# Kernel tuning notes

Measured on AMD Instinct MI355X. Metric: run time of the kernel, lower is better.

Reference implementation:

```python
import jax, jax.numpy as jnp
import numpy as np

N_USERS = 100_000
N_ITEMS = 50_000
N_EDGES = 2_000_000
D = 64
ALPHA = 0.5      # tanh-blend coefficient (alpha)
NORM_2 = -1.0    # exponent on back-aggregation degree norm (args.norm_2)


def setup_inputs() -> dict:
    key = jax.random.key(0)
    k1, k2, k3, k4, k5 = jax.random.split(key, 5)
    return {
        "h_user": jax.random.normal(k1, (N_USERS, D), jnp.float32) * 0.1,
        "pretrained_feature": jax.random.normal(k2, (N_ITEMS, D), jnp.float32),
        "edge_w": jax.random.normal(k3, (N_ITEMS, 1), jnp.float32),
        "src_idx": jax.random.randint(k4, (N_EDGES,), 0, N_USERS, dtype=jnp.int32),
        "dst_idx": jax.random.randint(k5, (N_EDGES,), 0, N_ITEMS, dtype=jnp.int32),
    }


def reference(h_user, pretrained_feature, edge_w, src_idx, dst_idx):
    # HGCNLayer.forward: bidirectional copy_src+sum aggregation with degree norm,
    # tanh prompt blend and node-softmax edge weighting.
    ones = jnp.ones((N_EDGES,), h_user.dtype)

    # forward pass user -> item: rst[d] = sum_{(s,d) in E} h_user[s]
    rst = jax.ops.segment_sum(h_user[src_idx], dst_idx, num_segments=N_ITEMS)  # [N_ITEMS, D]
    deg_dst = jnp.clip(jax.ops.segment_sum(ones, dst_idx, num_segments=N_ITEMS), 1.0)

    # alpha * tanh prompt blend
    rst = rst + ALPHA * jnp.tanh(pretrained_feature)
    # edge-prompt softmax scaling (softmax over nodes; see notes)
    rst = jax.nn.softmax(edge_w, axis=0) * rst
    # in-degree^-1 normalization
    rst = rst / deg_dst[:, None]

    # backward pass item -> user: bsrc[s] = sum_{(s,d) in E} rst[d]
    bsrc = jax.ops.segment_sum(rst[dst_idx], src_idx, num_segments=N_USERS)  # [N_USERS, D]
    deg_src = jnp.clip(jax.ops.segment_sum(ones, src_idx, num_segments=N_USERS), 1.0)
    bsrc = bsrc * jnp.power(deg_src, NORM_2)[:, None]
    return bsrc
```

## Files before the change

### kernel.cpp

```cpp
#include <hip/hip_runtime.h>
#include <hip/hip_bf16.h>
#include <math.h>

#define N_USERS 100000
#define N_ITEMS 50000
#define N_EDGES 2000000
#define D 64

#define FB_BINS 98
#define BB_BINS 196
#define NBINS   (FB_BINS + BB_BINS)
#define CHUNK   2048
#define NCHUNK  ((N_EDGES + CHUNK - 1) / CHUNK)
#define FINE_FWD (FB_BINS * 512)
#define FINE_ALL (FINE_FWD + BB_BINS * 512)
#define FWD_WGS ((N_ITEMS + 31) / 32)
#define BWD_WGS ((N_USERS + 31) / 32)

__device__ __forceinline__ float blo(unsigned u) {
    union { unsigned i; float f; } c; c.i = u << 16; return c.f;
}
__device__ __forceinline__ float bhi(unsigned u) {
    union { unsigned i; float f; } c; c.i = u & 0xFFFF0000u; return c.f;
}
__device__ __forceinline__ unsigned bpack(float x, float y) {
    __hip_bfloat16 a = __float2bfloat16(x), b = __float2bfloat16(y);
    unsigned short ua = *reinterpret_cast<unsigned short*>(&a);
    unsigned short ub = *reinterpret_cast<unsigned short*>(&b);
    return (unsigned)ua | ((unsigned)ub << 16);
}

__global__ __launch_bounds__(256) void h2b_kernel(
    const float2* __restrict__ in, unsigned* __restrict__ out, int n) {
    int stride = gridDim.x * blockDim.x;
    for (int i = blockIdx.x * blockDim.x + threadIdx.x; i < n; i += stride) {
        float2 v = in[i];
        out[i] = bpack(v.x, v.y);
    }
}

__global__ __launch_bounds__(256) void hist_kernel(
    const int* __restrict__ src, const int* __restrict__ dst, int* __restrict__ gh) {
    __shared__ int h[NBINS];
    for (int i = threadIdx.x; i < NBINS; i += 256) h[i] = 0;
    __syncthreads();
    int stride = gridDim.x * blockDim.x;
    for (int e = blockIdx.x * blockDim.x + threadIdx.x; e < N_EDGES; e += stride) {
        atomicAdd(&h[dst[e] >> 9], 1);
        atomicAdd(&h[FB_BINS + (src[e] >> 9)], 1);
    }
    __syncthreads();
    for (int i = threadIdx.x; i < NBINS; i += 256) {
        int v = h[i];
        if (v) atomicAdd(&gh[i], v);
    }
}

__global__ void scan_excl(const int* __restrict__ in, int* __restrict__ out,
                          int* __restrict__ cur, int n) {
    const int T = 1024, E = 4;
    __shared__ int wsum[16];
    __shared__ int s_carry;
    if (threadIdx.x == 0) s_carry = 0;
    __syncthreads();

    int lane = threadIdx.x & 63;
    int wid  = threadIdx.x >> 6;

    for (int base = 0; base < n; base += T * E) {
        int idx0 = base + threadIdx.x * E;
        int v[E];
        int tot = 0;
#pragma unroll
        for (int e = 0; e < E; e++) {
            int i = idx0 + e;
            v[e] = (i < n) ? in[i] : 0;
            tot += v[e];
        }
        int incl = tot;
#pragma unroll
        for (int off = 1; off < 64; off <<= 1) {
            int t = __shfl_up(incl, off);
            if (lane >= off) incl += t;
        }
        if (lane == 63) wsum[wid] = incl;
        __syncthreads();
        if (wid == 0 && lane < 16) {
            int t = wsum[lane];
            int sc = t;
#pragma unroll
            for (int off = 1; off < 16; off <<= 1) {
                int u = __shfl_up(sc, off);
                if (lane >= off) sc += u;
            }
            wsum[lane] = sc - t;
        }
        __syncthreads();
        int wave_off = wsum[wid];
        int excl = s_carry + wave_off + incl - tot;
#pragma unroll
        for (int e = 0; e < E; e++) {
            int i = idx0 + e;
            if (i < n) { out[i] = excl; cur[i] = excl; }
            excl += v[e];
        }
        __syncthreads();
        if (threadIdx.x == T - 1) s_carry += wave_off + incl;
        __syncthreads();
    }
    if (threadIdx.x == 0) out[n] = s_carry;
}

__global__ __launch_bounds__(256) void binfill_kernel(
    const int* __restrict__ src, const int* __restrict__ dst,
    int* __restrict__ gcur, unsigned* __restrict__ stage) {
    __shared__ int cnt[NBINS];
    __shared__ int gbase[NBINS];
    __shared__ int lcur[NBINS];
    int c = blockIdx.x;
    int base = c * CHUNK;
    int nEdge = N_EDGES - base; if (nEdge > CHUNK) nEdge = CHUNK;

    for (int t = threadIdx.x; t < NBINS; t += 256) { cnt[t] = 0; lcur[t] = 0; }
    __syncthreads();

    int es[8], ed[8];
#pragma unroll
    for (int j = 0; j < 8; j++) {
        int k = j * 256 + threadIdx.x;
        if (k < nEdge) {
            es[j] = src[base + k];
            ed[j] = dst[base + k];
            atomicAdd(&cnt[ed[j] >> 9], 1);
            atomicAdd(&cnt[FB_BINS + (es[j] >> 9)], 1);
        } else {
            es[j] = -1;
        }
    }
    __syncthreads();
    for (int t = threadIdx.x; t < NBINS; t += 256) {
        int cv = cnt[t];
        gbase[t] = cv ? atomicAdd(&gcur[t], cv) : 0;
    }
    __syncthreads();
#pragma unroll
    for (int j = 0; j < 8; j++) {
        if (es[j] >= 0) {
            int s = es[j], d = ed[j];
            int bf = d >> 9;
            int p = atomicAdd(&lcur[bf], 1);
            stage[gbase[bf] + p] = (unsigned)s | ((unsigned)(d & 511) << 17);
            int bb = FB_BINS + (s >> 9);
            int q = atomicAdd(&lcur[bb], 1);
            stage[gbase[bb] + q] = (unsigned)d | ((unsigned)(s & 511) << 16);
        }
    }
}

__global__ __launch_bounds__(512) void redist_kernel(
    const unsigned* __restrict__ stage, const int* __restrict__ binoff,
    unsigned* __restrict__ stage2, int* __restrict__ fineoff) {
    __shared__ int cnt[512];
    __shared__ int wsum[8];
    int B = blockIdx.x;
    int fwd = (B < FB_BINS) ? 1 : 0;
    int beg = binoff[B], end = binoff[B + 1];
    int tid = threadIdx.x, lane = tid & 63, wv = tid >> 6;
    int sh = fwd ? 17 : 16;
    unsigned pmask = fwd ? 0x1FFFFu : 0xFFFFu;

    cnt[tid] = 0;
    __syncthreads();
    for (int k = beg + tid; k < end; k += 512)
        atomicAdd(&cnt[(stage[k] >> sh) & 511], 1);
    __syncthreads();

    int v = cnt[tid];
    int incl = v;
#pragma unroll
    for (int off = 1; off < 64; off <<= 1) {
        int t = __shfl_up(incl, off);
        if (lane >= off) incl += t;
    }
    if (lane == 63) wsum[wv] = incl;
    __syncthreads();
    if (tid == 0) {
        int run = 0;
#pragma unroll
        for (int w = 0; w < 8; w++) { int t = wsum[w]; wsum[w] = run; run += t; }
    }
    __syncthreads();
    int excl = wsum[wv] + incl - v;

    int fbase = fwd ? (B * 512) : (FINE_FWD + (B - FB_BINS) * 512);
    fineoff[fbase + tid] = beg + excl;
    cnt[tid] = excl;
    __syncthreads();

    for (int k = beg + tid; k < end; k += 512) {
        unsigned e = stage[k];
        int lid = (e >> sh) & 511;
        int p = atomicAdd(&cnt[lid], 1);
        stage2[beg + p] = e & pmask;
    }
}

__global__ void softmax_stats_kernel(const float* __restrict__ w, float* __restrict__ stats) {
    __shared__ float red[16];
    int tid = threadIdx.x, lane = tid & 63, wid = tid >> 6;

    float m = -INFINITY;
    for (int i = tid; i < N_ITEMS; i += 1024) m = fmaxf(m, w[i]);
#pragma unroll
    for (int off = 32; off; off >>= 1) m = fmaxf(m, __shfl_xor(m, off));
    if (lane == 0) red[wid] = m;
    __syncthreads();
    if (tid == 0) {
        float t = red[0];
        for (int k = 1; k < 16; k++) t = fmaxf(t, red[k]);
        red[0] = t;
    }
    __syncthreads();
    m = red[0];
    __syncthreads();

    float s = 0.f;
    for (int i = tid; i < N_ITEMS; i += 1024) s += expf(w[i] - m);
#pragma unroll
    for (int off = 32; off; off >>= 1) s += __shfl_xor(s, off);
    if (lane == 0) red[wid] = s;
    __syncthreads();
    if (tid == 0) {
        float t = 0.f;
        for (int k = 0; k < 16; k++) t += red[k];
        stats[0] = m;
        stats[1] = t;
    }
}

__global__ __launch_bounds__(256) void pass2_fwd_kernel(
    const unsigned* __restrict__ hu16, const float* __restrict__ pf,
    const float* __restrict__ edge_w, const unsigned* __restrict__ stage2,
    const int* __restrict__ fineoff, const float* __restrict__ stats,
    unsigned* __restrict__ rst16) {
    int tid = threadIdx.x, lane = tid & 63, wv = tid >> 6;
    int q = lane & 31, half = lane >> 5;
    float m = stats[0], ssum = stats[1];
    const float2* PF2 = (const float2*)pf;
    int i0 = blockIdx.x * 32;

    for (int il = wv; il < 32; il += 4) {
        int i = i0 + il;
        if (i >= N_ITEMS) break;
        int a = fineoff[i], b = fineoff[i + 1];
        float ax = 0.f, ay = 0.f;
        int k = a;
        for (; k + 8 <= b; k += 8) {
            int s0 = (int)stage2[k + half],     s1 = (int)stage2[k + 2 + half];
            int s2 = (int)stage2[k + 4 + half], s3 = (int)stage2[k + 6 + half];
            unsigned u0 = hu16[(s0 << 5) + q];
            unsigned u1 = hu16[(s1 << 5) + q];
            unsigned u2 = hu16[(s2 << 5) + q];
            unsigned u3 = hu16[(s3 << 5) + q];
            ax += (blo(u0) + blo(u1)) + (blo(u2) + blo(u3));
            ay += (bhi(u0) + bhi(u1)) + (bhi(u2) + bhi(u3));
        }
        for (; k + 2 <= b; k += 2) {
            unsigned u = hu16[((int)stage2[k + half] << 5) + q];
            ax += blo(u); ay += bhi(u);
        }
        if (k < b && half == 0) {
            unsigned u = hu16[((int)stage2[k] << 5) + q];
            ax += blo(u); ay += bhi(u);
        }
        ax += __shfl_xor(ax, 32);
        ay += __shfl_xor(ay, 32);
        if (half == 0) {
            float deg = (float)(b - a);
            if (deg < 1.f) deg = 1.f;
            float sc = expf(edge_w[i] - m) / (ssum * deg);
            float2 pv = PF2[(size_t)i * 32 + q];
            float vx = (ax + 0.5f * tanhf(pv.x)) * sc;
            float vy = (ay + 0.5f * tanhf(pv.y)) * sc;
            rst16[(size_t)i * 32 + q] = bpack(vx, vy);
        }
    }
}

__global__ __launch_bounds__(256) void pass2_bwd_kernel(
    const unsigned* __restrict__ rst16, const unsigned* __restrict__ stage2,
    const int* __restrict__ fineoff, float* __restrict__ out) {
    int tid = threadIdx.x, lane = tid & 63, wv = tid >> 6;
    int q = lane & 31, half = lane >> 5;
    float2* OUT2 = (float2*)out;
    int u0i = blockIdx.x * 32;

    for (int il = wv; il < 32; il += 4) {
        int u = u0i + il;
        if (u >= N_USERS) break;
        int a = fineoff[FINE_FWD + u], b = fineoff[FINE_FWD + u + 1];
        float ax = 0.f, ay = 0.f;
        int k = a;
        for (; k + 8 <= b; k += 8) {
            int d0 = (int)stage2[k + half],     d1 = (int)stage2[k + 2 + half];
            int d2 = (int)stage2[k + 4 + half], d3 = (int)stage2[k + 6 + half];
            unsigned u0 = rst16[(d0 << 5) + q];
            unsigned u1 = rst16[(d1 << 5) + q];
            unsigned u2 = rst16[(d2 << 5) + q];
            unsigned u3 = rst16[(d3 << 5) + q];
            ax += (blo(u0) + blo(u1)) + (blo(u2) + blo(u3));
            ay += (bhi(u0) + bhi(u1)) + (bhi(u2) + bhi(u3));
        }
        for (; k + 2 <= b; k += 2) {
            unsigned e = rst16[((int)stage2[k + half] << 5) + q];
            ax += blo(e); ay += bhi(e);
        }
        if (k < b && half == 0) {
            unsigned e = rst16[((int)stage2[k] << 5) + q];
            ax += blo(e); ay += bhi(e);
        }
        ax += __shfl_xor(ax, 32);
        ay += __shfl_xor(ay, 32);
        if (half == 0) {
            float deg = (float)(b - a);
            if (deg < 1.f) deg = 1.f;
            OUT2[(size_t)u * 32 + q] = make_float2(ax / deg, ay / deg);
        }
    }
}

extern "C" void kernel_launch(void* const* d_in, const int* in_sizes, int n_in,
                              void* d_out, int out_size, void* d_ws, size_t ws_size,
                              hipStream_t stream) {
    const float* h_user = (const float*)d_in[0];
    const float* pf     = (const float*)d_in[1];
    const float* edge_w = (const float*)d_in[2];
    const int*   src    = (const int*)d_in[3];
    const int*   dst    = (const int*)d_in[4];
    float* out = (float*)d_out;

    char* p = (char*)d_ws;
    int* gh      = (int*)p;      p += sizeof(int) * NBINS;
    int* binoff  = (int*)p;      p += sizeof(int) * (NBINS + 1);
    int* gcur    = (int*)p;      p += sizeof(int) * NBINS;
    int* fineoff = (int*)p;      p += sizeof(int) * FINE_ALL;
    unsigned* stage  = (unsigned*)p; p += sizeof(unsigned) * (size_t)2 * N_EDGES;
    unsigned* stage2 = (unsigned*)p; p += sizeof(unsigned) * (size_t)2 * N_EDGES;
    unsigned* hu16   = (unsigned*)p; p += sizeof(unsigned) * (size_t)N_USERS * 32;
    unsigned* rst16  = (unsigned*)p; p += sizeof(unsigned) * (size_t)N_ITEMS * 32;
    float* stats = (float*)p;    p += 2 * sizeof(float);

    hipMemsetAsync(gh, 0, sizeof(int) * NBINS, stream);

    hist_kernel<<<256, 256, 0, stream>>>(src, dst, gh);
    scan_excl<<<1, 1024, 0, stream>>>(gh, binoff, gcur, NBINS);
    binfill_kernel<<<NCHUNK, 256, 0, stream>>>(src, dst, gcur, stage);
    redist_kernel<<<NBINS, 512, 0, stream>>>(stage, binoff, stage2, fineoff);
    h2b_kernel<<<1024, 256, 0, stream>>>((const float2*)h_user, hu16, N_USERS * 32);
    softmax_stats_kernel<<<1, 1024, 0, stream>>>(edge_w, stats);
    pass2_fwd_kernel<<<FWD_WGS, 256, 0, stream>>>(hu16, pf, edge_w, stage2, fineoff, stats, rst16);
    pass2_bwd_kernel<<<BWD_WGS, 256, 0, stream>>>(rst16, stage2, fineoff, out);
}
```

Before: 350.2 us.

## Build CSR via global per-node degree histogram and multi-block scan

Replaces the coarse bin histogram and the per-bin shared-memory redistribution with a global per-node degree count, computed with atomics and fused into the bf16 conversion kernel. A three-stage multi-block scan then produces the fine offsets directly. The redistribution kernel is split four ways per bin and uses global atomics on per-node cursors, which gives more parallelism than one workgroup per bin. The softmax stats are folded into the scan kernel, cutting launch count. The cost is heavy global atomic traffic on 150K counters in the prep pass and a large memset.

Measured after the change: 528.5 us. +50.9%, slower.

```diff
diff --git a/kernel.cpp b/kernel.cpp
--- a/kernel.cpp
+++ b/kernel.cpp
@@ -10,10 +10,15 @@
 #define FB_BINS 98
 #define BB_BINS 196
 #define NBINS   (FB_BINS + BB_BINS)
+#define NBINS_P8 296
 #define CHUNK   2048
 #define NCHUNK  ((N_EDGES + CHUNK - 1) / CHUNK)
 #define FINE_FWD (FB_BINS * 512)
-#define FINE_ALL (FINE_FWD + BB_BINS * 512)
+#define FINE_TOT (NBINS * 512)
+#define SCAN_BLK 4096
+#define SCAN_WGS 37
+#define FINE_PAD (SCAN_WGS * SCAN_BLK)
+#define TOTSLOT  (2 * N_EDGES)
 #define FWD_WGS ((N_ITEMS + 31) / 32)
 #define BWD_WGS ((N_USERS + 31) / 32)
 
@@ -30,85 +35,127 @@
     return (unsigned)ua | ((unsigned)ub << 16);
 }
 
-__global__ __launch_bounds__(256) void h2b_kernel(
-    const float2* __restrict__ in, unsigned* __restrict__ out, int n) {
+__global__ __launch_bounds__(256) void prep_kernel(
+    const float2* __restrict__ hin, unsigned* __restrict__ hu16,
+    const int* __restrict__ src, const int* __restrict__ dst,
+    int* __restrict__ deg) {
     int stride = gridDim.x * blockDim.x;
-    for (int i = blockIdx.x * blockDim.x + threadIdx.x; i < n; i += stride) {
-        float2 v = in[i];
-        out[i] = bpack(v.x, v.y);
-    }
-}
-
-__global__ __launch_bounds__(256) void hist_kernel(
-    const int* __restrict__ src, const int* __restrict__ dst, int* __restrict__ gh) {
-    __shared__ int h[NBINS];
-    for (int i = threadIdx.x; i < NBINS; i += 256) h[i] = 0;
-    __syncthreads();
-    int stride = gridDim.x * blockDim.x;
-    for (int e = blockIdx.x * blockDim.x + threadIdx.x; e < N_EDGES; e += stride) {
-        atomicAdd(&h[dst[e] >> 9], 1);
-        atomicAdd(&h[FB_BINS + (src[e] >> 9)], 1);
-    }
-    __syncthreads();
-    for (int i = threadIdx.x; i < NBINS; i += 256) {
-        int v = h[i];
-        if (v) atomicAdd(&gh[i], v);
-    }
-}
-
-__global__ void scan_excl(const int* __restrict__ in, int* __restrict__ out,
-                          int* __restrict__ cur, int n) {
-    const int T = 1024, E = 4;
-    __shared__ int wsum[16];
-    __shared__ int s_carry;
-    if (threadIdx.x == 0) s_carry = 0;
-    __syncthreads();
-
-    int lane = threadIdx.x & 63;
-    int wid  = threadIdx.x >> 6;
-
-    for (int base = 0; base < n; base += T * E) {
-        int idx0 = base + threadIdx.x * E;
-        int v[E];
-        int tot = 0;
-#pragma unroll
-        for (int e = 0; e < E; e++) {
-            int i = idx0 + e;
-            v[e] = (i < n) ? in[i] : 0;
-            tot += v[e];
-        }
-        int incl = tot;
-#pragma unroll
-        for (int off = 1; off < 64; off <<= 1) {
-            int t = __shfl_up(incl, off);
-            if (lane >= off) incl += t;
-        }
-        if (lane == 63) wsum[wid] = incl;
-        __syncthreads();
-        if (wid == 0 && lane < 16) {
-            int t = wsum[lane];
-            int sc = t;
-#pragma unroll
-            for (int off = 1; off < 16; off <<= 1) {
-                int u = __shfl_up(sc, off);
-                if (lane >= off) sc += u;
+    int t0 = blockIdx.x * blockDim.x + threadIdx.x;
+    for (int i = t0; i < N_USERS * 32; i += stride) {
+        float2 v = hin[i];
+        hu16[i] = bpack(v.x, v.y);
+    }
+    for (int e = t0; e < N_EDGES; e += stride) {
+        atomicAdd(&deg[dst[e]], 1);
+        atomicAdd(&deg[FINE_FWD + src[e]], 1);
+    }
+}
+
+__global__ __launch_bounds__(256) void scanA_kernel(
+    const int* __restrict__ deg, int* __restrict__ blocksum) {
+    __shared__ int ws[4];
+    int b = blockIdx.x, t = threadIdx.x, lane = t & 63, wv = t >> 6;
+    const int4* Dp = (const int4*)(deg + b * SCAN_BLK);
+    int s = 0;
+#pragma unroll
+    for (int j = 0; j < 4; j++) {
+        int4 v = Dp[t * 4 + j];
+        s += v.x + v.y + v.z + v.w;
+    }
+#pragma unroll
+    for (int off = 32; off; off >>= 1) s += __shfl_xor(s, off);
+    if (lane == 0) ws[wv] = s;
+    __syncthreads();
+    if (t == 0) blocksum[b] = ws[0] + ws[1] + ws[2] + ws[3];
+}
+
+__global__ void scanB_kernel(const int* __restrict__ blocksum, int* __restrict__ blockbase,
+                             const float* __restrict__ w, float* __restrict__ stats) {
+    __shared__ float red[16];
+    if (blockIdx.x == 0) {
+        int t = threadIdx.x;
+        if (t < 64) {
+            int v = (t < SCAN_WGS) ? blocksum[t] : 0;
+            int incl = v;
+#pragma unroll
+            for (int off = 1; off < 64; off <<= 1) {
+                int u = __shfl_up(incl, off);
+                if (t >= off) incl += u;
             }
-            wsum[lane] = sc - t;
-        }
-        __syncthreads();
-        int wave_off = wsum[wid];
-        int excl = s_carry + wave_off + incl - tot;
-#pragma unroll
-        for (int e = 0; e < E; e++) {
-            int i = idx0 + e;
-            if (i < n) { out[i] = excl; cur[i] = excl; }
-            excl += v[e];
-        }
-        __syncthreads();
-        if (threadIdx.x == T - 1) s_carry += wave_off + incl;
-        __syncthreads();
-    }
-    if (threadIdx.x == 0) out[n] = s_carry;
+            if (t < SCAN_WGS) blockbase[t] = incl - v;
+        }
+        return;
+    }
+    int tid = threadIdx.x, lane = tid & 63, wid = tid >> 6;
+
+    float m = -INFINITY;
+    for (int i = tid; i < N_ITEMS; i += 1024) m = fmaxf(m, w[i]);
+#pragma unroll
+    for (int off = 32; off; off >>= 1) m = fmaxf(m, __shfl_xor(m, off));
+    if (lane == 0) red[wid] = m;
+    __syncthreads();
+    if (tid == 0) {
+        float t = red[0];
+        for (int k = 1; k < 16; k++) t = fmaxf(t, red[k]);
+        red[0] = t;
+    }
+    __syncthreads();
+    m = red[0];
+    __syncthreads();
+
+    float s = 0.f;
+    for (int i = tid; i < N_ITEMS; i += 1024) s += expf(w[i] - m);
+#pragma unroll
+    for (int off = 32; off; off >>= 1) s += __shfl_xor(s, off);
+    if (lane == 0) red[wid] = s;
+    __syncthreads();
+    if (tid == 0) {
+        float t = 0.f;
+        for (int k = 0; k < 16; k++) t += red[k];
+        stats[0] = m;
+        stats[1] = t;
+    }
+}
+
+__global__ __launch_bounds__(256) void scanC_kernel(
+    const int* __restrict__ blockbase, int* deg_cur,
+    int* __restrict__ fineoff, int* __restrict__ gcur) {
+    __shared__ int wbase[4];
+    int b = blockIdx.x, t = threadIdx.x, lane = t & 63, wv = t >> 6;
+    int4 v[4];
+    const int4* Dp = (const int4*)(deg_cur + b * SCAN_BLK);
+#pragma unroll
+    for (int j = 0; j < 4; j++) v[j] = Dp[t * 4 + j];
+    int tot = 0;
+#pragma unroll
+    for (int j = 0; j < 4; j++) tot += v[j].x + v[j].y + v[j].z + v[j].w;
+    int incl = tot;
+#pragma unroll
+    for (int off = 1; off < 64; off <<= 1) {
+        int u = __shfl_up(incl, off);
+        if (lane >= off) incl += u;
+    }
+    if (lane == 63) wbase[wv] = incl;
+    __syncthreads();
+    if (t == 0) {
+        int run = 0;
+#pragma unroll
+        for (int k = 0; k < 4; k++) { int x = wbase[k]; wbase[k] = run; run += x; }
+    }
+    __syncthreads();
+    int base = blockbase[b] + wbase[wv] + incl - tot;
+    int idx0 = b * SCAN_BLK + t * 16;
+#pragma unroll
+    for (int j = 0; j < 4; j++) {
+        int c0 = v[j].x, c1 = v[j].y, c2 = v[j].z, c3 = v[j].w;
+        int i = idx0 + j * 4;
+        fineoff[i] = base; deg_cur[i] = base;
+        if ((i & 511) == 0 && (i >> 9) < NBINS) gcur[i >> 9] = base;
+        base += c0;
+        fineoff[i + 1] = base; deg_cur[i + 1] = base; base += c1;
+        fineoff[i + 2] = base; deg_cur[i + 2] = base; base += c2;
+        fineoff[i + 3] = base; deg_cur[i + 3] = base; base += c3;
+    }
 }
 
 __global__ __launch_bounds__(256) void binfill_kernel(
@@ -157,84 +204,30 @@
     }
 }
 
-__global__ __launch_bounds__(512) void redist_kernel(
-    const unsigned* __restrict__ stage, const int* __restrict__ binoff,
-    unsigned* __restrict__ stage2, int* __restrict__ fineoff) {
-    __shared__ int cnt[512];
-    __shared__ int wsum[8];
-    int B = blockIdx.x;
-    int fwd = (B < FB_BINS) ? 1 : 0;
-    int beg = binoff[B], end = binoff[B + 1];
-    int tid = threadIdx.x, lane = tid & 63, wv = tid >> 6;
-    int sh = fwd ? 17 : 16;
-    unsigned pmask = fwd ? 0x1FFFFu : 0xFFFFu;
-
-    cnt[tid] = 0;
-    __syncthreads();
-    for (int k = beg + tid; k < end; k += 512)
-        atomicAdd(&cnt[(stage[k] >> sh) & 511], 1);
-    __syncthreads();
-
-    int v = cnt[tid];
-    int incl = v;
-#pragma unroll
-    for (int off = 1; off < 64; off <<= 1) {
-        int t = __shfl_up(incl, off);
-        if (lane >= off) incl += t;
-    }
-    if (lane == 63) wsum[wv] = incl;
-    __syncthreads();
-    if (tid == 0) {
-        int run = 0;
-#pragma unroll
-        for (int w = 0; w < 8; w++) { int t = wsum[w]; wsum[w] = run; run += t; }
-    }
-    __syncthreads();
-    int excl = wsum[wv] + incl - v;
-
-    int fbase = fwd ? (B * 512) : (FINE_FWD + (B - FB_BINS) * 512);
-    fineoff[fbase + tid] = beg + excl;
-    cnt[tid] = excl;
-    __syncthreads();
-
-    for (int k = beg + tid; k < end; k += 512) {
-        unsigned e = stage[k];
-        int lid = (e >> sh) & 511;
-        int p = atomicAdd(&cnt[lid], 1);
-        stage2[beg + p] = e & pmask;
-    }
-}
-
-__global__ void softmax_stats_kernel(const float* __restrict__ w, float* __restrict__ stats) {
-    __shared__ float red[16];
-    int tid = threadIdx.x, lane = tid & 63, wid = tid >> 6;
-
-    float m = -INFINITY;
-    for (int i = tid; i < N_ITEMS; i += 1024) m = fmaxf(m, w[i]);
-#pragma unroll
-    for (int off = 32; off; off >>= 1) m = fmaxf(m, __shfl_xor(m, off));
-    if (lane == 0) red[wid] = m;
-    __syncthreads();
-    if (tid == 0) {
-        float t = red[0];
-        for (int k = 1; k < 16; k++) t = fmaxf(t, red[k]);
-        red[0] = t;
-    }
-    __syncthreads();
-    m = red[0];
-    __syncthreads();
-
-    float s = 0.f;
-    for (int i = tid; i < N_ITEMS; i += 1024) s += expf(w[i] - m);
-#pragma unroll
-    for (int off = 32; off; off >>= 1) s += __shfl_xor(s, off);
-    if (lane == 0) red[wid] = s;
-    __syncthreads();
-    if (tid == 0) {
-        float t = 0.f;
-        for (int k = 0; k < 16; k++) t += red[k];
-        stats[0] = m;
-        stats[1] = t;
+__global__ __launch_bounds__(256) void redist2_kernel(
+    const unsigned* __restrict__ stage, const int* __restrict__ fineoff,
+    int* __restrict__ cur, unsigned* __restrict__ stage2) {
+    int x = blockIdx.x;
+    int B = x % NBINS_P8, s4 = x / NBINS_P8;
+    if (B >= NBINS) return;
+    int beg = fineoff[B << 9], end = fineoff[(B + 1) << 9];
+    int n = end - beg;
+    int q0 = beg + ((n * s4) >> 2), q1 = beg + ((n * (s4 + 1)) >> 2);
+    int t = threadIdx.x;
+    if (B < FB_BINS) {
+        for (int k = q0 + t; k < q1; k += 256) {
+            unsigned e = stage[k];
+            int gid = (B << 9) | (int)(e >> 17);
+            int p = atomicAdd(&cur[gid], 1);
+            stage2[p] = e & 0x1FFFFu;
+        }
+    } else {
+        for (int k = q0 + t; k < q1; k += 256) {
+            unsigned e = stage[k];
+            int gid = (B << 9) | (int)(e >> 16);
+            int p = atomicAdd(&cur[gid], 1);
+            stage2[p] = e & 0xFFFFu;
+        }
     }
 }
 
@@ -340,24 +333,25 @@
     float* out = (float*)d_out;
 
     char* p = (char*)d_ws;
-    int* gh      = (int*)p;      p += sizeof(int) * NBINS;
-    int* binoff  = (int*)p;      p += sizeof(int) * (NBINS + 1);
-    int* gcur    = (int*)p;      p += sizeof(int) * NBINS;
-    int* fineoff = (int*)p;      p += sizeof(int) * FINE_ALL;
-    unsigned* stage  = (unsigned*)p; p += sizeof(unsigned) * (size_t)2 * N_EDGES;
-    unsigned* stage2 = (unsigned*)p; p += sizeof(unsigned) * (size_t)2 * N_EDGES;
+    int* deg      = (int*)p;     p += sizeof(int) * FINE_PAD;
+    int* fineoff  = (int*)p;     p += sizeof(int) * FINE_PAD;
+    int* gcur     = (int*)p;     p += sizeof(int) * NBINS_P8;
+    int* blocksum = (int*)p;     p += sizeof(int) * 64;
+    int* blockbase= (int*)p;     p += sizeof(int) * 64;
+    unsigned* stage  = (unsigned*)p; p += sizeof(unsigned) * (size_t)TOTSLOT;
+    unsigned* stage2 = (unsigned*)p; p += sizeof(unsigned) * (size_t)TOTSLOT;
     unsigned* hu16   = (unsigned*)p; p += sizeof(unsigned) * (size_t)N_USERS * 32;
     unsigned* rst16  = (unsigned*)p; p += sizeof(unsigned) * (size_t)N_ITEMS * 32;
-    float* stats = (float*)p;    p += 2 * sizeof(float);
-
-    hipMemsetAsync(gh, 0, sizeof(int) * NBINS, stream);
-
-    hist_kernel<<<256, 256, 0, stream>>>(src, dst, gh);
-    scan_excl<<<1, 1024, 0, stream>>>(gh, binoff, gcur, NBINS);
+    float* stats = (float*)p;    p += 4 * sizeof(float);
+
+    hipMemsetAsync(deg, 0, sizeof(int) * FINE_PAD, stream);
+
+    prep_kernel<<<1024, 256, 0, stream>>>((const float2*)h_user, hu16, src, dst, deg);
+    scanA_kernel<<<SCAN_WGS, 256, 0, stream>>>(deg, blocksum);
+    scanB_kernel<<<2, 1024, 0, stream>>>(blocksum, blockbase, edge_w, stats);
+    scanC_kernel<<<SCAN_WGS, 256, 0, stream>>>(blockbase, deg, fineoff, gcur);
     binfill_kernel<<<NCHUNK, 256, 0, stream>>>(src, dst, gcur, stage);
-    redist_kernel<<<NBINS, 512, 0, stream>>>(stage, binoff, stage2, fineoff);
-    h2b_kernel<<<1024, 256, 0, stream>>>((const float2*)h_user, hu16, N_USERS * 32);
-    softmax_stats_kernel<<<1, 1024, 0, stream>>>(edge_w, stats);
+    redist2_kernel<<<4 * NBINS_P8, 256, 0, stream>>>(stage, fineoff, deg, stage2);
     pass2_fwd_kernel<<<FWD_WGS, 256, 0, stream>>>(hu16, pf, edge_w, stage2, fineoff, stats, rst16);
     pass2_bwd_kernel<<<BWD_WGS, 256, 0, stream>>>(rst16, stage2, fineoff, out);
 }
```

## Split forward gather into source-sharded partial sums with a combine pass

Applied to the files above, without the earlier changes.

The forward user-to-item aggregation now sub-buckets each item's edges by the low two bits of the source index. Four separate workgroup groups each gather one shard into bf16 partial buffers, and a second kernel combines the partials and applies the tanh blend, softmax scale and degree normalisation. The redistribution kernel is reworked to build these sharded offsets, and the backward bins are processed two per workgroup. Index stream loads become nontemporal. The aim is better cache locality on the user embedding gathers, at the cost of an extra kernel, partial-sum traffic and an added bf16 rounding of the partials.

Result: slower. 398.1 us (+13.7%).

```diff
diff --git a/kernel.cpp b/kernel.cpp
--- a/kernel.cpp
+++ b/kernel.cpp
@@ -12,9 +12,13 @@
 #define NBINS   (FB_BINS + BB_BINS)
 #define CHUNK   2048
 #define NCHUNK  ((N_EDGES + CHUNK - 1) / CHUNK)
-#define FINE_FWD (FB_BINS * 512)
-#define FINE_ALL (FINE_FWD + BB_BINS * 512)
-#define FWD_WGS ((N_ITEMS + 31) / 32)
+#define NSH     4
+#define FOFF_F_N (FB_BINS * 512 * NSH + 1)
+#define FOFF_B_N (BB_BINS * 512 + 1)
+#define TOTSLOT  (2 * N_EDGES)
+#define PART_SLOTS (FB_BINS * 512 * NSH)
+#define PASSA_WGS (((N_ITEMS + 31) / 32) * 8)
+#define PASSB_WGS ((N_ITEMS + 7) / 8)
 #define BWD_WGS ((N_USERS + 31) / 32)
 
 __device__ __forceinline__ float blo(unsigned u) {
@@ -157,51 +161,94 @@
     }
 }
 
-__global__ __launch_bounds__(512) void redist_kernel(
+__global__ __launch_bounds__(512) void redist3_kernel(
     const unsigned* __restrict__ stage, const int* __restrict__ binoff,
-    unsigned* __restrict__ stage2, int* __restrict__ fineoff) {
-    __shared__ int cnt[512];
+    unsigned* __restrict__ stage2, int* __restrict__ foff_f, int* __restrict__ foff_b) {
+    __shared__ int cnt[512 * NSH];
     __shared__ int wsum[8];
-    int B = blockIdx.x;
-    int fwd = (B < FB_BINS) ? 1 : 0;
-    int beg = binoff[B], end = binoff[B + 1];
-    int tid = threadIdx.x, lane = tid & 63, wv = tid >> 6;
-    int sh = fwd ? 17 : 16;
-    unsigned pmask = fwd ? 0x1FFFFu : 0xFFFFu;
-
-    cnt[tid] = 0;
-    __syncthreads();
-    for (int k = beg + tid; k < end; k += 512)
-        atomicAdd(&cnt[(stage[k] >> sh) & 511], 1);
-    __syncthreads();
-
-    int v = cnt[tid];
-    int incl = v;
-#pragma unroll
-    for (int off = 1; off < 64; off <<= 1) {
-        int t = __shfl_up(incl, off);
-        if (lane >= off) incl += t;
-    }
-    if (lane == 63) wsum[wv] = incl;
-    __syncthreads();
-    if (tid == 0) {
-        int run = 0;
-#pragma unroll
-        for (int w = 0; w < 8; w++) { int t = wsum[w]; wsum[w] = run; run += t; }
-    }
-    __syncthreads();
-    int excl = wsum[wv] + incl - v;
-
-    int fbase = fwd ? (B * 512) : (FINE_FWD + (B - FB_BINS) * 512);
-    fineoff[fbase + tid] = beg + excl;
-    cnt[tid] = excl;
-    __syncthreads();
-
-    for (int k = beg + tid; k < end; k += 512) {
-        unsigned e = stage[k];
-        int lid = (e >> sh) & 511;
-        int p = atomicAdd(&cnt[lid], 1);
-        stage2[beg + p] = e & pmask;
+    int wg = blockIdx.x, t = threadIdx.x, lane = t & 63, wv = t >> 6;
+
+    if (wg < FB_BINS) {
+        int B = wg;
+        int beg = binoff[B], end = binoff[B + 1];
+        for (int j = t; j < 512 * NSH; j += 512) cnt[j] = 0;
+        __syncthreads();
+        for (int k = beg + t; k < end; k += 512) {
+            unsigned e = stage[k];
+            atomicAdd(&cnt[(((e >> 17) & 511) << 2) | (e & 3)], 1);
+        }
+        __syncthreads();
+        int c[NSH]; int tot = 0;
+#pragma unroll
+        for (int j = 0; j < NSH; j++) { c[j] = cnt[(t << 2) | j]; tot += c[j]; }
+        int incl = tot;
+#pragma unroll
+        for (int off = 1; off < 64; off <<= 1) {
+            int u = __shfl_up(incl, off);
+            if (lane >= off) incl += u;
+        }
+        if (lane == 63) wsum[wv] = incl;
+        __syncthreads();
+        if (t == 0) {
+            int run = 0;
+#pragma unroll
+            for (int k2 = 0; k2 < 8; k2++) { int x = wsum[k2]; wsum[k2] = run; run += x; }
+        }
+        __syncthreads();
+        int base = beg + wsum[wv] + incl - tot;
+        int slot0 = (((B << 9) | t) << 2);
+#pragma unroll
+        for (int j = 0; j < NSH; j++) {
+            foff_f[slot0 + j] = base;
+            cnt[(t << 2) | j] = base;
+            base += c[j];
+        }
+        if (B == FB_BINS - 1 && t == 0) foff_f[FB_BINS * 512 * NSH] = end;
+        __syncthreads();
+        for (int k = beg + t; k < end; k += 512) {
+            unsigned e = stage[k];
+            int idx = (((e >> 17) & 511) << 2) | (e & 3);
+            int p = atomicAdd(&cnt[idx], 1);
+            stage2[p] = e & 0x1FFFFu;
+        }
+    } else {
+        for (int pass = 0; pass < 2; pass++) {
+            int B = FB_BINS + ((wg - FB_BINS) << 1) + pass;
+            int beg = binoff[B], end = binoff[B + 1];
+            cnt[t] = 0;
+            __syncthreads();
+            for (int k = beg + t; k < end; k += 512) {
+                unsigned e = stage[k];
+                atomicAdd(&cnt[(e >> 16) & 511], 1);
+            }
+            __syncthreads();
+            int v = cnt[t];
+            int incl = v;
+#pragma unroll
+            for (int off = 1; off < 64; off <<= 1) {
+                int u = __shfl_up(incl, off);
+                if (lane >= off) incl += u;
+            }
+            if (lane == 63) wsum[wv] = incl;
+            __syncthreads();
+            if (t == 0) {
+                int run = 0;
+#pragma unroll
+                for (int k2 = 0; k2 < 8; k2++) { int x = wsum[k2]; wsum[k2] = run; run += x; }
+            }
+            __syncthreads();
+            int base = beg + wsum[wv] + incl - v;
+            foff_b[((B - FB_BINS) << 9) | t] = base;
+            cnt[t] = base;
+            if (B == NBINS - 1 && t == 0) foff_b[BB_BINS * 512] = end;
+            __syncthreads();
+            for (int k = beg + t; k < end; k += 512) {
+                unsigned e = stage[k];
+                int p = atomicAdd(&cnt[(e >> 16) & 511], 1);
+                stage2[p] = e & 0xFFFFu;
+            }
+            __syncthreads();
+        }
     }
 }
 
@@ -238,26 +285,27 @@
     }
 }
 
-__global__ __launch_bounds__(256) void pass2_fwd_kernel(
-    const unsigned* __restrict__ hu16, const float* __restrict__ pf,
-    const float* __restrict__ edge_w, const unsigned* __restrict__ stage2,
-    const int* __restrict__ fineoff, const float* __restrict__ stats,
-    unsigned* __restrict__ rst16) {
+__global__ __launch_bounds__(256) void passA_fwd_kernel(
+    const unsigned* __restrict__ hu16, const unsigned* __restrict__ stage2,
+    const int* __restrict__ foff_f, unsigned* __restrict__ part) {
     int tid = threadIdx.x, lane = tid & 63, wv = tid >> 6;
     int q = lane & 31, half = lane >> 5;
-    float m = stats[0], ssum = stats[1];
-    const float2* PF2 = (const float2*)pf;
-    int i0 = blockIdx.x * 32;
-
-    for (int il = wv; il < 32; il += 4) {
+    int ib = blockIdx.x >> 3, x = blockIdx.x & 7;
+    int sh = x >> 1, hb = x & 1;
+    int i0 = ib * 32 + hb * 16;
+
+    for (int il = wv; il < 16; il += 4) {
         int i = i0 + il;
         if (i >= N_ITEMS) break;
-        int a = fineoff[i], b = fineoff[i + 1];
+        int slot = (i << 2) | sh;
+        int a = foff_f[slot], b = foff_f[slot + 1];
         float ax = 0.f, ay = 0.f;
         int k = a;
         for (; k + 8 <= b; k += 8) {
-            int s0 = (int)stage2[k + half],     s1 = (int)stage2[k + 2 + half];
-            int s2 = (int)stage2[k + 4 + half], s3 = (int)stage2[k + 6 + half];
+            int s0 = (int)__builtin_nontemporal_load(&stage2[k + half]);
+            int s1 = (int)__builtin_nontemporal_load(&stage2[k + 2 + half]);
+            int s2 = (int)__builtin_nontemporal_load(&stage2[k + 4 + half]);
+            int s3 = (int)__builtin_nontemporal_load(&stage2[k + 6 + half]);
             unsigned u0 = hu16[(s0 << 5) + q];
             unsigned u1 = hu16[(s1 << 5) + q];
             unsigned u2 = hu16[(s2 << 5) + q];
@@ -266,30 +314,48 @@
             ay += (bhi(u0) + bhi(u1)) + (bhi(u2) + bhi(u3));
         }
         for (; k + 2 <= b; k += 2) {
-            unsigned u = hu16[((int)stage2[k + half] << 5) + q];
+            unsigned u = hu16[((int)__builtin_nontemporal_load(&stage2[k + half]) << 5) + q];
             ax += blo(u); ay += bhi(u);
         }
         if (k < b && half == 0) {
-            unsigned u = hu16[((int)stage2[k] << 5) + q];
+            unsigned u = hu16[((int)__builtin_nontemporal_load(&stage2[k]) << 5) + q];
             ax += blo(u); ay += bhi(u);
         }
         ax += __shfl_xor(ax, 32);
         ay += __shfl_xor(ay, 32);
-        if (half == 0) {
-            float deg = (float)(b - a);
-            if (deg < 1.f) deg = 1.f;
-            float sc = expf(edge_w[i] - m) / (ssum * deg);
-            float2 pv = PF2[(size_t)i * 32 + q];
-            float vx = (ax + 0.5f * tanhf(pv.x)) * sc;
-            float vy = (ay + 0.5f * tanhf(pv.y)) * sc;
-            rst16[(size_t)i * 32 + q] = bpack(vx, vy);
-        }
-    }
+        if (half == 0)
+            __builtin_nontemporal_store(bpack(ax, ay), &part[((size_t)slot << 5) + q]);
+    }
+}
+
+__global__ __launch_bounds__(256) void passB_fwd_kernel(
+    const unsigned* __restrict__ part, const float* __restrict__ pf,
+    const float* __restrict__ edge_w, const int* __restrict__ foff_f,
+    const float* __restrict__ stats, unsigned* __restrict__ rst16) {
+    int tid = threadIdx.x, lane = tid & 63, wv = tid >> 6;
+    int q = lane & 31, half = lane >> 5;
+    int i = blockIdx.x * 8 + wv * 2 + half;
+    if (i >= N_ITEMS) return;
+    float m = stats[0], ssum = stats[1];
+    float ax = 0.f, ay = 0.f;
+#pragma unroll
+    for (int s = 0; s < NSH; s++) {
+        unsigned u = __builtin_nontemporal_load(&part[(((size_t)(i << 2) | s) << 5) + q]);
+        ax += blo(u); ay += bhi(u);
+    }
+    int dg = foff_f[(i << 2) + 4] - foff_f[i << 2];
+    float deg = dg < 1 ? 1.f : (float)dg;
+    float sc = expf(edge_w[i] - m) / (ssum * deg);
+    const float2* PF2 = (const float2*)pf;
+    float2 pv = PF2[(size_t)i * 32 + q];
+    float vx = (ax + 0.5f * tanhf(pv.x)) * sc;
+    float vy = (ay + 0.5f * tanhf(pv.y)) * sc;
+    rst16[(size_t)i * 32 + q] = bpack(vx, vy);
 }
 
 __global__ __launch_bounds__(256) void pass2_bwd_kernel(
     const unsigned* __restrict__ rst16, const unsigned* __restrict__ stage2,
-    const int* __restrict__ fineoff, float* __restrict__ out) {
+    const int* __restrict__ foff_b, float* __restrict__ out) {
     int tid = threadIdx.x, lane = tid & 63, wv = tid >> 6;
     int q = lane & 31, half = lane >> 5;
     float2* OUT2 = (float2*)out;
@@ -298,12 +364,14 @@
     for (int il = wv; il < 32; il += 4) {
         int u = u0i + il;
         if (u >= N_USERS) break;
-        int a = fineoff[FINE_FWD + u], b = fineoff[FINE_FWD + u + 1];
+        int a = foff_b[u], b = foff_b[u + 1];
         float ax = 0.f, ay = 0.f;
         int k = a;
         for (; k + 8 <= b; k += 8) {
-            int d0 = (int)stage2[k + half],     d1 = (int)stage2[k + 2 + half];
-            int d2 = (int)stage2[k + 4 + half], d3 = (int)stage2[k + 6 + half];
+            int d0 = (int)__builtin_nontemporal_load(&stage2[k + half]);
+            int d1 = (int)__builtin_nontemporal_load(&stage2[k + 2 + half]);
+            int d2 = (int)__builtin_nontemporal_load(&stage2[k + 4 + half]);
+            int d3 = (int)__builtin_nontemporal_load(&stage2[k + 6 + half]);
             unsigned u0 = rst16[(d0 << 5) + q];
             unsigned u1 = rst16[(d1 << 5) + q];
             unsigned u2 = rst16[(d2 << 5) + q];
@@ -312,11 +380,11 @@
             ay += (bhi(u0) + bhi(u1)) + (bhi(u2) + bhi(u3));
         }
         for (; k + 2 <= b; k += 2) {
-            unsigned e = rst16[((int)stage2[k + half] << 5) + q];
+            unsigned e = rst16[((int)__builtin_nontemporal_load(&stage2[k + half]) << 5) + q];
             ax += blo(e); ay += bhi(e);
         }
         if (k < b && half == 0) {
-            unsigned e = rst16[((int)stage2[k] << 5) + q];
+            unsigned e = rst16[((int)__builtin_nontemporal_load(&stage2[k]) << 5) + q];
             ax += blo(e); ay += bhi(e);
         }
         ax += __shfl_xor(ax, 32);
@@ -340,24 +408,28 @@
     float* out = (float*)d_out;
 
     char* p = (char*)d_ws;
-    int* gh      = (int*)p;      p += sizeof(int) * NBINS;
-    int* binoff  = (int*)p;      p += sizeof(int) * (NBINS + 1);
-    int* gcur    = (int*)p;      p += sizeof(int) * NBINS;
-    int* fineoff = (int*)p;      p += sizeof(int) * FINE_ALL;
-    unsigned* stage  = (unsigned*)p; p += sizeof(unsigned) * (size_t)2 * N_EDGES;
-    unsigned* stage2 = (unsigned*)p; p += sizeof(unsigned) * (size_t)2 * N_EDGES;
+    int* gh      = (int*)p;     p += sizeof(int) * NBINS;
+    int* binoff  = (int*)p;     p += sizeof(int) * (NBINS + 1);
+    int* gcur    = (int*)p;     p += sizeof(int) * NBINS;
+    int* foff_f  = (int*)p;     p += sizeof(int) * FOFF_F_N;
+    int* foff_b  = (int*)p;     p += sizeof(int) * FOFF_B_N;
+    float* stats = (float*)p;   p += 4 * sizeof(float);
+    unsigned* part  = (unsigned*)p;
+    unsigned* stage = part;
+    p += sizeof(unsigned) * (size_t)PART_SLOTS * 32;
+    unsigned* stage2 = (unsigned*)p; p += sizeof(unsigned) * (size_t)TOTSLOT;
     unsigned* hu16   = (unsigned*)p; p += sizeof(unsigned) * (size_t)N_USERS * 32;
     unsigned* rst16  = (unsigned*)p; p += sizeof(unsigned) * (size_t)N_ITEMS * 32;
-    float* stats = (float*)p;    p += 2 * sizeof(float);
 
     hipMemsetAsync(gh, 0, sizeof(int) * NBINS, stream);
 
     hist_kernel<<<256, 256, 0, stream>>>(src, dst, gh);
     scan_excl<<<1, 1024, 0, stream>>>(gh, binoff, gcur, NBINS);
     binfill_kernel<<<NCHUNK, 256, 0, stream>>>(src, dst, gcur, stage);
-    redist_kernel<<<NBINS, 512, 0, stream>>>(stage, binoff, stage2, fineoff);
+    redist3_kernel<<<196, 512, 0, stream>>>(stage, binoff, stage2, foff_f, foff_b);
     h2b_kernel<<<1024, 256, 0, stream>>>((const float2*)h_user, hu16, N_USERS * 32);
     softmax_stats_kernel<<<1, 1024, 0, stream>>>(edge_w, stats);
-    pass2_fwd_kernel<<<FWD_WGS, 256, 0, stream>>>(hu16, pf, edge_w, stage2, fineoff, stats, rst16);
-    pass2_bwd_kernel<<<BWD_WGS, 256, 0, stream>>>(rst16, stage2, fineoff, out);
-}
+    passA_fwd_kernel<<<PASSA_WGS, 256, 0, stream>>>(hu16, stage2, foff_f, part);
+    passB_fwd_kernel<<<PASSB_WGS, 256, 0, stream>>>(part, pf, edge_w, foff_f, stats, rst16);
+    pass2_bwd_kernel<<<BWD_WGS, 256, 0, stream>>>(rst16, stage2, foff_b, out);
+}
```
